# Performance work log

Hardware: AMD Instinct MI355X
Metric: run time of the kernel (lower is better)

## Reference

```python
import jax, jax.numpy as jnp
import numpy as np

B, S, C = 4, 2048, 1024

def setup_inputs() -> dict:
    key = jax.random.key(0)
    ks = jax.random.split(key, 9)
    lim = 1.0 / np.sqrt(C)  # torch nn.Linear default init range
    def lin_params(kw, kb):
        W = jax.random.uniform(kw, (C, C), jnp.float32, -lim, lim)
        b = jax.random.uniform(kb, (C,), jnp.float32, -lim, lim)
        return W, b
    Wq, bq = lin_params(ks[0], ks[1])
    Wk, bk = lin_params(ks[2], ks[3])
    Wv, bv = lin_params(ks[4], ks[5])
    query = jax.random.normal(ks[6], (B, S, C), jnp.float32)
    key_t = jax.random.normal(ks[7], (B, S, C), jnp.float32)
    value = jax.random.normal(ks[8], (B, S, C), jnp.float32)
    return {"query": query, "key": key_t, "value": value,
            "Wq": Wq, "bq": bq, "Wk": Wk, "bk": bk, "Wv": Wv, "bv": bv}

def reference(query, key, value, Wq, bq, Wk, bk, Wv, bv):
    # Linear projections: y = x @ W^T + b (torch Linear convention, W is [out, in])
    Q = jnp.einsum('bsc,dc->bsd', query, Wq) + bq
    K = jnp.einsum('bsc,dc->bsd', key, Wk) + bk
    V = jnp.einsum('bsc,dc->bsd', value, Wv) + bv
    scale = jnp.float32(C) ** 0.5
    scores = jnp.einsum('bqd,bkd->bqk', Q, K) / scale  # [B, S, S]
    attn = jax.nn.softmax(scores, axis=-1)
    out = jnp.einsum('bqk,bkd->bqd', attn, V)  # [B, S, C]
    return out
```

## Files before the change

kernel.cpp:

```cpp
#include <hip/hip_runtime.h>
#include <hip/hip_bf16.h>


typedef _Float16 half8 __attribute__((ext_vector_type(8)));
typedef _Float16 half4 __attribute__((ext_vector_type(4)));
typedef float f32x4 __attribute__((ext_vector_type(4)));

#define AS1(p) ((const __attribute__((address_space(1))) void*)(p))
#define AS3(p) ((__attribute__((address_space(3))) void*)(p))
#define MFMA16(a, b, c) __builtin_amdgcn_mfma_f32_16x16x32_f16(a, b, c, 0, 0, 0)

__global__ __launch_bounds__(256) void cvt6_f32_f16(
    const float* __restrict__ q, const float* __restrict__ k,
    const float* __restrict__ v, const float* __restrict__ wq,
    const float* __restrict__ wk, const float* __restrict__ wv,
    _Float16* __restrict__ Xq, _Float16* __restrict__ Wqh) {
    constexpr long XSZ = 8388608, WSZ = 1048576;
    const int b = blockIdx.x;
    const float* s;
    _Float16* d;
    long i;
    if (b < 12288) {
        const int tz = b >> 12;
        s = tz == 0 ? q : tz == 1 ? k : v;
        d = Xq + (long)tz * XSZ;
        i = (long)(b & 4095) * 2048 + threadIdx.x * 8;
    } else {
        const int b2 = b - 12288;
        const int tz = b2 >> 9;
        s = tz == 0 ? wq : tz == 1 ? wk : wv;
        d = Wqh + (long)tz * WSZ;
        i = (long)(b2 & 511) * 2048 + threadIdx.x * 8;
    }
    float4 a = *(const float4*)(s + i);
    float4 c = *(const float4*)(s + i + 4);
    half8 h;
    h[0] = (_Float16)a.x; h[1] = (_Float16)a.y; h[2] = (_Float16)a.z; h[3] = (_Float16)a.w;
    h[4] = (_Float16)c.x; h[5] = (_Float16)c.y; h[6] = (_Float16)c.z; h[7] = (_Float16)c.w;
    *(half8*)(d + i) = h;
}

__global__ __launch_bounds__(256, 2)
void gemm_proj(const _Float16* __restrict__ A, const _Float16* __restrict__ Bt,
               const float* __restrict__ b0, const float* __restrict__ b1,
               const float* __restrict__ b2, _Float16* __restrict__ QKout,
               _Float16* __restrict__ VtOut) {
    constexpr int K = 1024;
    __shared__ _Float16 Asm[128 * 64] __attribute__((aligned(16)));
    __shared__ _Float16 Bsm[128 * 64] __attribute__((aligned(16)));
    const int tid = threadIdx.x;
    const int lane = tid & 63;
    const int wave = tid >> 6;

    const int lin = blockIdx.x;
    const int g = lin & 7;
    const int s = lin >> 3;
    const int xt = s & 7;
    const int row_id = g * 24 + (s >> 3);
    const int yt = row_id & 63;
    const int tz = row_id >> 6;
    const int m0 = yt * 128;
    const int n0 = xt * 128;

    const float* bias = tz == 0 ? b0 : tz == 1 ? b1 : b2;
    const _Float16* Abase = A + (long)tz * 8388608 + (long)m0 * K;
    const _Float16* Bbase = Bt + (long)tz * 1048576 + (long)n0 * K;

    const int srow8 = lane >> 3;
    const int sq = ((lane & 7) ^ srow8) << 3;
    const int quad = lane >> 4;
    const int l16 = lane & 15;
    const int wm = (wave >> 1) << 6;
    const int wn = (wave & 1) << 6;
    const int fa0 = (wm + l16) * 64 + (((0 * 4 + quad) ^ (l16 & 7)) << 3);
    const int fa1 = (wm + l16) * 64 + (((1 * 4 + quad) ^ (l16 & 7)) << 3);
    const int fb0 = (wn + l16) * 64 + (((0 * 4 + quad) ^ (l16 & 7)) << 3);
    const int fb1 = (wn + l16) * 64 + (((1 * 4 + quad) ^ (l16 & 7)) << 3);

    f32x4 acc[4][4];
#pragma unroll
    for (int i = 0; i < 4; i++)
#pragma unroll
        for (int j = 0; j < 4; j++)
#pragma unroll
            for (int r = 0; r < 4; r++) acc[i][j][r] = 0.0f;

    for (int k0 = 0; k0 < K; k0 += 64) {
        __syncthreads();
#pragma unroll
        for (int u = 0; u < 8; ++u) {
            const int t = wave + u * 4;
            if (t < 16) {
                __builtin_amdgcn_global_load_lds(
                    AS1(Abase + (long)(t * 8 + srow8) * K + k0 + sq),
                    AS3(Asm + t * 512), 16, 0, 0);
            } else {
                __builtin_amdgcn_global_load_lds(
                    AS1(Bbase + (long)((t - 16) * 8 + srow8) * K + k0 + sq),
                    AS3(Bsm + (t - 16) * 512), 16, 0, 0);
            }
        }
        __syncthreads();

#pragma unroll
        for (int ks = 0; ks < 2; ++ks) {
            const int ao = ks ? fa1 : fa0;
            const int bo = ks ? fb1 : fb0;
            half8 af[4], bf[4];
#pragma unroll
            for (int i = 0; i < 4; i++) af[i] = *(const half8*)(Asm + ao + i * 1024);
#pragma unroll
            for (int j = 0; j < 4; j++) bf[j] = *(const half8*)(Bsm + bo + j * 1024);
#pragma unroll
            for (int i = 0; i < 4; i++)
#pragma unroll
                for (int j = 0; j < 4; j++)
                    acc[i][j] = MFMA16(af[i], bf[j], acc[i][j]);
        }
    }

    const bool trout = (tz == 2);
#pragma unroll
    for (int i = 0; i < 4; i++) {
        const int row = m0 + wm + i * 16 + quad * 4;
#pragma unroll
        for (int j = 0; j < 4; j++) {
            const int col = n0 + wn + j * 16 + l16;
            const float badd = bias[col];
            if (trout) {
                const long b = row >> 11;
                const int sl = row & 2047;
                half4 h;
#pragma unroll
                for (int r = 0; r < 4; r++) h[r] = (_Float16)(acc[i][j][r] + badd);
                *(half4*)(VtOut + b * 2097152 + (long)col * 2048 + sl) = h;
            } else {
                _Float16* o = QKout + (long)tz * 8388608;
#pragma unroll
                for (int r = 0; r < 4; r++)
                    o[(long)(row + r) * 1024 + col] = (_Float16)(acc[i][j][r] + badd);
            }
        }
    }
}

template <int K, int NX_SH, int R, int NYT_SH, bool F16OUT>
__global__ __launch_bounds__(256, 2)
void gemm_nt(const _Float16* __restrict__ A, const _Float16* __restrict__ Bt,
             void* __restrict__ Cout, int N, float scale,
             long sA, long sB, long sC) {
    __shared__ _Float16 Asm[128 * 128] __attribute__((aligned(16)));
    __shared__ _Float16 Bsm[128 * 128] __attribute__((aligned(16)));
    const int tid = threadIdx.x;
    const int lane = tid & 63;
    const int wave = tid >> 6;

    const int lin = blockIdx.x;
    const int g = lin & 7;
    const int s = lin >> 3;
    const int xt = s & ((1 << NX_SH) - 1);
    const int row_id = g * R + (s >> NX_SH);
    const int yt = row_id & ((1 << NYT_SH) - 1);
    const int tz = row_id >> NYT_SH;
    const int m0 = yt * 128;
    const int n0 = xt * 128;

    A += (long)tz * sA;
    Bt += (long)tz * sB;

    const int rin = lane >> 4;
    const int pch = lane & 15;
    const int quad = lane >> 4;
    const int l16 = lane & 15;
    const int wm = (wave >> 1) << 6;
    const int wn = (wave & 1) << 6;
    const int fa_base = (wm + l16) * 128;
    const int fb_base = (wn + l16) * 128;
    int ch[4];
#pragma unroll
    for (int ks = 0; ks < 4; ++ks) ch[ks] = (((ks * 4 + quad) ^ l16) << 3);

    f32x4 acc[4][4];
#pragma unroll
    for (int i = 0; i < 4; i++)
#pragma unroll
        for (int j = 0; j < 4; j++)
#pragma unroll
            for (int r = 0; r < 4; r++) acc[i][j][r] = 0.0f;

    const _Float16* Abase = A + (long)m0 * K;
    const _Float16* Bbase = Bt + (long)n0 * K;

    for (int k0 = 0; k0 < K; k0 += 128) {
        __syncthreads();
#pragma unroll
        for (int u = 0; u < 16; ++u) {
            const int t = wave + u * 4;
            const int sl = t & 31;
            const int r = sl * 4 + rin;
            const int lq = (pch ^ (((sl & 3) << 2) + rin)) << 3;
            if (t < 32) {
                __builtin_amdgcn_global_load_lds(
                    AS1(Abase + (long)r * K + k0 + lq),
                    AS3(Asm + sl * 512), 16, 0, 0);
            } else {
                __builtin_amdgcn_global_load_lds(
                    AS1(Bbase + (long)r * K + k0 + lq),
                    AS3(Bsm + sl * 512), 16, 0, 0);
            }
        }
        __syncthreads();

#pragma unroll
        for (int ks = 0; ks < 4; ++ks) {
            half8 af[4], bf[4];
#pragma unroll
            for (int i = 0; i < 4; i++) af[i] = *(const half8*)(Asm + fa_base + i * 2048 + ch[ks]);
#pragma unroll
            for (int j = 0; j < 4; j++) bf[j] = *(const half8*)(Bsm + fb_base + j * 2048 + ch[ks]);
#pragma unroll
            for (int i = 0; i < 4; i++)
#pragma unroll
                for (int j = 0; j < 4; j++)
                    acc[i][j] = MFMA16(af[i], bf[j], acc[i][j]);
        }
    }

#pragma unroll
    for (int i = 0; i < 4; i++) {
        const int row = m0 + wm + i * 16 + quad * 4;
#pragma unroll
        for (int j = 0; j < 4; j++) {
            const int col = n0 + wn + j * 16 + l16;
#pragma unroll
            for (int r = 0; r < 4; r++) {
                float v = acc[i][j][r] * scale;
                if constexpr (F16OUT)
                    ((_Float16*)Cout + (long)tz * sC)[(long)(row + r) * N + col] = (_Float16)v;
                else
                    ((float*)Cout + (long)tz * sC)[(long)(row + r) * N + col] = v;
            }
        }
    }
}

__global__ __launch_bounds__(256) void softmax4_f16(const _Float16* __restrict__ S,
                                                    _Float16* __restrict__ P) {
    const int wave = threadIdx.x >> 6;
    const int lane = threadIdx.x & 63;
    const long row = (long)blockIdx.x * 4 + wave;
    const _Float16* src = S + row * 2048;
    _Float16* dst = P + row * 2048;

    half8 h[4];
#pragma unroll
    for (int u = 0; u < 4; u++) h[u] = ((const half8*)src)[lane + 64 * u];
    float v[32];
#pragma unroll
    for (int u = 0; u < 4; u++)
#pragma unroll
        for (int j = 0; j < 8; j++) v[u * 8 + j] = (float)h[u][j];

    float m = v[0];
#pragma unroll
    for (int e = 1; e < 32; e++) m = fmaxf(m, v[e]);
#pragma unroll
    for (int off = 32; off > 0; off >>= 1) m = fmaxf(m, __shfl_xor(m, off, 64));

    float sum = 0.0f;
#pragma unroll
    for (int e = 0; e < 32; e++) { v[e] = __expf(v[e] - m); sum += v[e]; }
#pragma unroll
    for (int off = 32; off > 0; off >>= 1) sum += __shfl_xor(sum, off, 64);
    const float inv = 1.0f / sum;

#pragma unroll
    for (int u = 0; u < 4; u++) {
        half8 o;
#pragma unroll
        for (int j = 0; j < 8; j++) o[j] = (_Float16)(v[u * 8 + j] * inv);
        ((half8*)dst)[lane + 64 * u] = o;
    }
}

extern "C" void kernel_launch(void* const* d_in, const int* in_sizes, int n_in,
                              void* d_out, int out_size, void* d_ws, size_t ws_size,
                              hipStream_t stream) {
    constexpr int B = 4, S = 2048, C = 1024;
    constexpr long XSZ = (long)B * S * C;

    const float* query = (const float*)d_in[0];
    const float* key   = (const float*)d_in[1];
    const float* value = (const float*)d_in[2];
    const float* Wq = (const float*)d_in[3];
    const float* bq = (const float*)d_in[4];
    const float* Wk = (const float*)d_in[5];
    const float* bk = (const float*)d_in[6];
    const float* Wv = (const float*)d_in[7];
    const float* bv = (const float*)d_in[8];
    float* out = (float*)d_out;
    char* ws = (char*)d_ws;

    _Float16* Xq  = (_Float16*)(ws + 0);
    _Float16* Wqh = (_Float16*)(ws + 3 * XSZ * 2);
    _Float16* scores = (_Float16*)(ws + 0);
    _Float16* Qh  = (_Float16*)(ws + 73400320);
    _Float16* attn = (_Float16*)(ws + 73400320);
    _Float16* Vt  = (_Float16*)(ws + 106954752);
    if (ws_size < 123731968) return;

    cvt6_f32_f16<<<13824, 256, 0, stream>>>(
        query, key, value, Wq, Wk, Wv, Xq, Wqh);

    gemm_proj<<<1536, 256, 0, stream>>>(
        Xq, Wqh, bq, bk, bv, Qh, Vt);

    gemm_nt<1024, 4, 8, 4, true><<<1024, 256, 0, stream>>>(
        Qh, Qh + XSZ, scores, S, 0.03125f,
        (long)S * C, (long)S * C, (long)S * S);

    softmax4_f16<<<B * S / 4, 256, 0, stream>>>(scores, attn);

    gemm_nt<2048, 3, 8, 4, false><<<512, 256, 0, stream>>>(
        attn, Vt, out, C, 1.0f,
        (long)S * S, (long)C * S, (long)S * C);
}
```

Baseline: 299.5 us.

## Fuse fp32-to-fp16 activation conversion into projection GEMM A-tile loads

The separate conversion pass over query/key/value is removed. The projection GEMM now reads fp32 activations directly, converts them in registers, and writes swizzled fp16 tiles to LDS, while weights are still pre-converted and loaded via global_load_lds. This avoids writing and rereading about 48MB of fp16 intermediates, at the cost of synchronous register-path loads in the GEMM main loop. Launch bounds are raised to 3 blocks per CU to help hide that extra load latency.

```diff
diff --git a/kernel.cpp b/kernel.cpp
--- a/kernel.cpp
+++ b/kernel.cpp
@@ -10,28 +10,15 @@
 #define AS3(p) ((__attribute__((address_space(3))) void*)(p))
 #define MFMA16(a, b, c) __builtin_amdgcn_mfma_f32_16x16x32_f16(a, b, c, 0, 0, 0)
 
-__global__ __launch_bounds__(256) void cvt6_f32_f16(
-    const float* __restrict__ q, const float* __restrict__ k,
-    const float* __restrict__ v, const float* __restrict__ wq,
-    const float* __restrict__ wk, const float* __restrict__ wv,
-    _Float16* __restrict__ Xq, _Float16* __restrict__ Wqh) {
-    constexpr long XSZ = 8388608, WSZ = 1048576;
+__global__ __launch_bounds__(256) void cvtw_f32_f16(
+    const float* __restrict__ wq, const float* __restrict__ wk,
+    const float* __restrict__ wv, _Float16* __restrict__ Wqh) {
+    constexpr long WSZ = 1048576;
     const int b = blockIdx.x;
-    const float* s;
-    _Float16* d;
-    long i;
-    if (b < 12288) {
-        const int tz = b >> 12;
-        s = tz == 0 ? q : tz == 1 ? k : v;
-        d = Xq + (long)tz * XSZ;
-        i = (long)(b & 4095) * 2048 + threadIdx.x * 8;
-    } else {
-        const int b2 = b - 12288;
-        const int tz = b2 >> 9;
-        s = tz == 0 ? wq : tz == 1 ? wk : wv;
-        d = Wqh + (long)tz * WSZ;
-        i = (long)(b2 & 511) * 2048 + threadIdx.x * 8;
-    }
+    const int tz = b >> 9;
+    const float* s = tz == 0 ? wq : tz == 1 ? wk : wv;
+    _Float16* d = Wqh + (long)tz * WSZ;
+    const long i = (long)(b & 511) * 2048 + threadIdx.x * 8;
     float4 a = *(const float4*)(s + i);
     float4 c = *(const float4*)(s + i + 4);
     half8 h;
@@ -40,11 +27,12 @@
     *(half8*)(d + i) = h;
 }
 
-__global__ __launch_bounds__(256, 2)
-void gemm_proj(const _Float16* __restrict__ A, const _Float16* __restrict__ Bt,
-               const float* __restrict__ b0, const float* __restrict__ b1,
-               const float* __restrict__ b2, _Float16* __restrict__ QKout,
-               _Float16* __restrict__ VtOut) {
+__global__ __launch_bounds__(256, 3)
+void gemm_projf(const float* __restrict__ X0, const float* __restrict__ X1,
+                const float* __restrict__ X2, const _Float16* __restrict__ Wh,
+                const float* __restrict__ b0, const float* __restrict__ b1,
+                const float* __restrict__ b2, _Float16* __restrict__ QKout,
+                _Float16* __restrict__ VtOut) {
     constexpr int K = 1024;
     __shared__ _Float16 Asm[128 * 64] __attribute__((aligned(16)));
     __shared__ _Float16 Bsm[128 * 64] __attribute__((aligned(16)));
@@ -62,12 +50,14 @@
     const int m0 = yt * 128;
     const int n0 = xt * 128;
 
+    const float* Xp = tz == 0 ? X0 : tz == 1 ? X1 : X2;
     const float* bias = tz == 0 ? b0 : tz == 1 ? b1 : b2;
-    const _Float16* Abase = A + (long)tz * 8388608 + (long)m0 * K;
-    const _Float16* Bbase = Bt + (long)tz * 1048576 + (long)n0 * K;
+    const float* Abase = Xp + (long)m0 * K;
+    const _Float16* Bbase = Wh + (long)tz * 1048576 + (long)n0 * K;
 
     const int srow8 = lane >> 3;
-    const int sq = ((lane & 7) ^ srow8) << 3;
+    const int scc = ((lane & 7) ^ srow8) << 3;
+    const int sqB = scc;
     const int quad = lane >> 4;
     const int l16 = lane & 15;
     const int wm = (wave >> 1) << 6;
@@ -88,17 +78,29 @@
     for (int k0 = 0; k0 < K; k0 += 64) {
         __syncthreads();
 #pragma unroll
-        for (int u = 0; u < 8; ++u) {
+        for (int u = 0; u < 4; ++u) {
             const int t = wave + u * 4;
-            if (t < 16) {
-                __builtin_amdgcn_global_load_lds(
-                    AS1(Abase + (long)(t * 8 + srow8) * K + k0 + sq),
-                    AS3(Asm + t * 512), 16, 0, 0);
-            } else {
-                __builtin_amdgcn_global_load_lds(
-                    AS1(Bbase + (long)((t - 16) * 8 + srow8) * K + k0 + sq),
-                    AS3(Bsm + (t - 16) * 512), 16, 0, 0);
-            }
+            __builtin_amdgcn_global_load_lds(
+                AS1(Bbase + (long)(t * 8 + srow8) * K + k0 + sqB),
+                AS3(Bsm + t * 512), 16, 0, 0);
+        }
+        float4 xa[4][2];
+#pragma unroll
+        for (int u = 0; u < 4; ++u) {
+            const int sl = wave + u * 4;
+            const float* src = Abase + (long)(sl * 8 + srow8) * K + k0 + scc;
+            xa[u][0] = *(const float4*)(src);
+            xa[u][1] = *(const float4*)(src + 4);
+        }
+#pragma unroll
+        for (int u = 0; u < 4; ++u) {
+            const int sl = wave + u * 4;
+            half8 h;
+            h[0] = (_Float16)xa[u][0].x; h[1] = (_Float16)xa[u][0].y;
+            h[2] = (_Float16)xa[u][0].z; h[3] = (_Float16)xa[u][0].w;
+            h[4] = (_Float16)xa[u][1].x; h[5] = (_Float16)xa[u][1].y;
+            h[6] = (_Float16)xa[u][1].z; h[7] = (_Float16)xa[u][1].w;
+            *(half8*)(Asm + sl * 512 + lane * 8) = h;
         }
         __syncthreads();
 
@@ -301,19 +303,17 @@
     float* out = (float*)d_out;
     char* ws = (char*)d_ws;
 
-    _Float16* Xq  = (_Float16*)(ws + 0);
-    _Float16* Wqh = (_Float16*)(ws + 3 * XSZ * 2);
+    _Float16* Wqh = (_Float16*)(ws + 50331648);
     _Float16* scores = (_Float16*)(ws + 0);
     _Float16* Qh  = (_Float16*)(ws + 73400320);
     _Float16* attn = (_Float16*)(ws + 73400320);
     _Float16* Vt  = (_Float16*)(ws + 106954752);
     if (ws_size < 123731968) return;
 
-    cvt6_f32_f16<<<13824, 256, 0, stream>>>(
-        query, key, value, Wq, Wk, Wv, Xq, Wqh);
-
-    gemm_proj<<<1536, 256, 0, stream>>>(
-        Xq, Wqh, bq, bk, bv, Qh, Vt);
+    cvtw_f32_f16<<<1536, 256, 0, stream>>>(Wq, Wk, Wv, Wqh);
+
+    gemm_projf<<<1536, 256, 0, stream>>>(
+        query, key, value, Wqh, bq, bk, bv, Qh, Vt);
 
     gemm_nt<1024, 4, 8, 4, true><<<1024, 256, 0, stream>>>(
         Qh, Qh + XSZ, scores, S, 0.03125f,
```

After: 363.9 us. 21.5% more time.
